# Performance work log

Measured on AMD Instinct MI355X. Metric: run time of the kernel, lower is better.

## Reference

```python
import jax, jax.numpy as jnp
import numpy as np

B, N, D_FEAT = 16, 1024, 64
NPOINT, RADIUS, NSAMPLE = 512, 0.2, 32
EPS = 1e-5


def _square_distance(src, dst):
    # src [b,S,3], dst [b,N,3] -> [b,S,N]
    d = -2.0 * jnp.einsum('bsc,bnc->bsn', src, dst)
    d = d + jnp.sum(src * src, -1)[:, :, None]
    d = d + jnp.sum(dst * dst, -1)[:, None, :]
    return d


def _fps(xyz, npoint):
    # xyz [b,N,3] -> indices [b,npoint]; seeded by point farthest from the mean
    b, n, _ = xyz.shape
    centroid = jnp.mean(xyz, axis=1, keepdims=True)
    distance = jnp.minimum(jnp.full((b, n), 1e10, xyz.dtype),
                           jnp.sum((xyz - centroid) ** 2, -1))
    farthest = jnp.argmax(distance, -1)
    bidx = jnp.arange(b)

    def body(carry, _):
        dist, far = carry
        c = xyz[bidx[:, None], far[:, None]]  # [b,1,3]
        dist = jnp.minimum(dist, jnp.sum((xyz - c) ** 2, -1))
        return (dist, jnp.argmax(dist, -1)), far

    _, idx = jax.lax.scan(body, (distance, farthest), None, length=npoint)
    return idx.T  # [b, npoint]


def _gather(points, idx):
    # points [b,N,C], idx [b,...] -> [b,...,C]
    return jax.vmap(lambda p, i: p[i])(points, idx)


def _query_ball(radius, nsample, xyz, new_xyz):
    # faithful to torch: mask out-of-radius with N, full sort, take first nsample,
    # replace sentinels by the first (closest-index) in-ball point
    b, n, _ = xyz.shape
    sqr = _square_distance(new_xyz, xyz)  # [b,S,N]
    idx = jnp.where(sqr > radius ** 2, n, jnp.arange(n)[None, None, :])
    idx = jnp.sort(idx, axis=-1)[:, :, :nsample]
    first = idx[:, :, :1]
    return jnp.where(idx == n, first, idx)


def _qbn(x):
    # QBN_RM training mode: divide by per-channel RMS of detached activations
    mean = jnp.mean(jax.lax.stop_gradient(x) ** 2, axis=(0, 2, 3))
    return x / jnp.sqrt(mean + EPS)[None, :, None, None]


def _qrelu(x):
    # scale each 3-vector by mod / max(mod, 1), coefficient detached
    b3, c, s, k = x.shape
    b = b3 // 3
    xd = jax.lax.stop_gradient(x).reshape(b, 3, c, s, k)
    mod = jnp.sqrt(jnp.sum(xd * xd, axis=1))  # [b,c,s,k]
    coeff = mod / jnp.maximum(mod, 1.0)
    return jnp.broadcast_to(coeff[:, None], (b, 3, c, s, k)).reshape(b3, c, s, k) * x


def _qmaxpool(x):
    # our_mpool1d with kernel (1, nsample): pick the max-modulus sample over K,
    # gather the same index for all 3 quaternion components
    b3, c, s, k = x.shape
    b = b3 // 3
    x5 = x.reshape(b, 3, c, s, k)
    mod = jnp.sum(jax.lax.stop_gradient(x5) ** 2, axis=1)  # argmax of mod == argmax of mod^2
    idx = jnp.argmax(mod, axis=-1)  # [b,c,s]
    idxb = jnp.broadcast_to(idx[:, None, :, :, None], (b, 3, c, s, 1))
    y = jnp.take_along_axis(x5, idxb, axis=-1)[..., 0]  # [b,3,c,s]
    return y.reshape(b3, c, s)


def setup_inputs() -> dict:
    key = jax.random.key(0)
    k1, k2, k3, k4, k5 = jax.random.split(key, 5)
    xyz = jax.random.normal(k1, (B, 3, N), dtype=jnp.float32)
    points = jax.random.normal(k2, (B * 3, D_FEAT, N), dtype=jnp.float32)
    W0 = jax.random.normal(k3, (64, 66), dtype=jnp.float32) * np.sqrt(2.0 / 66)
    W1 = jax.random.normal(k4, (64, 64), dtype=jnp.float32) * np.sqrt(2.0 / 64)
    W2 = jax.random.normal(k5, (128, 64), dtype=jnp.float32) * np.sqrt(2.0 / 64)
    return {"xyz": xyz, "points": points, "W0": W0, "W1": W1, "W2": W2}


def reference(xyz, points, W0, W1, W2):
    xyz_t = xyz.transpose(0, 2, 1)      # [B,N,3]
    pts_t = points.transpose(0, 2, 1)   # [B*3,N,D]

    fps_idx = _fps(xyz_t, NPOINT)                       # [B,S]
    new_xyz = _gather(xyz_t, fps_idx)                   # [B,S,3]
    idx = _query_ball(RADIUS, NSAMPLE, xyz_t, new_xyz)  # [B,S,K]

    g_xyz = _gather(xyz_t, idx)                         # [B,S,K,3]
    g_norm = g_xyz - new_xyz[:, :, None, :]
    gx = g_xyz.transpose(0, 3, 1, 2).reshape(B * 3, NPOINT, NSAMPLE, 1)
    gn = g_norm.transpose(0, 3, 1, 2).reshape(B * 3, NPOINT, NSAMPLE, 1)
    idx3 = jnp.broadcast_to(idx[:, None], (B, 3, NPOINT, NSAMPLE)).reshape(B * 3, NPOINT, NSAMPLE)
    gp = _gather(pts_t, idx3)                           # [B*3,S,K,D]

    x = jnp.concatenate([gn, gx, gp], axis=-1)          # [B*3,S,K,D+2]
    x = x.transpose(0, 3, 1, 2)                         # [B*3,D+2,S,K]
    for W in (W0, W1, W2):
        x = jnp.einsum('bcsk,oc->bosk', x, W)           # 1x1 conv, no bias
        x = _qrelu(_qbn(x))
    new_feat = _qmaxpool(x)                             # [B*3,128,S]
    return new_xyz.transpose(0, 2, 1), new_feat
```

## Files before the change

### kernel.cpp

```cpp
#include <hip/hip_runtime.h>

typedef unsigned int u32;
typedef unsigned long long u64;
typedef float v2f __attribute__((ext_vector_type(2)));

#define NB 16
#define NPT 1024
#define NP 512
#define NS 32
#define DF 64
#define RAD2 0.04f
#define EPSQ 1e-5f
#define CNTF 786432.0f
#define NGRP 8192
#define TCAP 96
#define TSLOT 128
#define NTILE_MAX 2731

__device__ __forceinline__ float rmul(float a, float b){ return __fmul_rn(a,b); }
__device__ __forceinline__ float radd(float a, float b){ return __fadd_rn(a,b); }
__device__ __forceinline__ float sq3(float a, float b, float c){
  return radd(radd(rmul(a,a), rmul(b,b)), rmul(c,c));
}

__device__ __forceinline__ float wave_sum64(float v){
  #pragma unroll
  for(int m=1;m<64;m<<=1) v += __shfl_xor(v, m, 64);
  return v;
}

__device__ __forceinline__ float half_sum32(float v){
  #pragma unroll
  for(int m=1;m<32;m<<=1) v += __shfl_xor(v, m, 64);
  return v;
}

#define DPPK(CTRL) do{ \
  unsigned _lo = (unsigned)k, _hi = (unsigned)(k>>32); \
  unsigned _mlo = (unsigned)__builtin_amdgcn_mov_dpp((int)_lo, (CTRL), 0xF, 0xF, true); \
  unsigned _mhi = (unsigned)__builtin_amdgcn_mov_dpp((int)_hi, (CTRL), 0xF, 0xF, true); \
  u64 _mk = ((u64)_mhi<<32) | _mlo; \
  k = (_mk > k) ? _mk : k; \
}while(0)

template<int PT>
__global__ __launch_bounds__(256) void fps_combo(const float* __restrict__ xyz,
                                                 float* __restrict__ out0,
                                                 const float* __restrict__ pts,
                                                 float* __restrict__ ptsT,
                                                 u32* __restrict__ witem){
#pragma clang fp contract(off)
  const int bid = blockIdx.x;
  const int t = threadIdx.x;
  if(bid >= 8){
    const int gid = (bid - 8)*256 + t;
    if(gid < NTILE_MAX*TSLOT) witem[gid] = 0xFFFFFFFFu;
    if constexpr(PT){
      const int w = gid >> 6, ln = gid & 63;
      if(w < 48*16){
        const int b3 = w >> 4, n0 = (w & 15) << 6;
        const float* src = pts + (((size_t)b3*64 + ln) << 10);
        float* dst = ptsT + (((size_t)b3*1024 + n0) << 6) + ln;
        #pragma unroll 4
        for(int i=0;i<64;i++) dst[(size_t)i << 6] = src[n0 + i];
      }
    }
    return;
  }
  __shared__ float4 plds[2048];
  if(t >= 64) return;
  const int lane = t;
  const int half = lane >> 5;
  const int hl   = lane & 31;
  const int b    = 2*bid + half;
  const float* xb = xyz + b*3*NPT;

  v2f px2[16], py2[16], pz2[16], dist2[16];
  u32 loj[32];
  #pragma unroll
  for(int i=0;i<16;i++){
    const int n0 = 64*i + hl, n1 = n0 + 32;
    float x0v = xb[n0],        x1v = xb[n1];
    float y0v = xb[NPT+n0],    y1v = xb[NPT+n1];
    float z0v = xb[2*NPT+n0],  z1v = xb[2*NPT+n1];
    px2[i].x = x0v; px2[i].y = x1v;
    py2[i].x = y0v; py2[i].y = y1v;
    pz2[i].x = z0v; pz2[i].y = z1v;
    loj[2*i]   = 1023u - (u32)n0;
    loj[2*i+1] = 1023u - (u32)n1;
    plds[(half<<10) + n0] = make_float4(x0v, y0v, z0v, 0.f);
    plds[(half<<10) + n1] = make_float4(x1v, y1v, z1v, 0.f);
  }
  float sx=0.f, sy=0.f, sz=0.f;
  #pragma unroll
  for(int i=0;i<16;i++){
    sx += px2[i].x; sx += px2[i].y;
    sy += py2[i].x; sy += py2[i].y;
    sz += pz2[i].x; sz += pz2[i].y;
  }
  sx = half_sum32(sx); sy = half_sum32(sy); sz = half_sum32(sz);
  const float cx = sx/1024.f, cy = sy/1024.f, cz = sz/1024.f;
  {
    v2f cx2; cx2.x=cx; cx2.y=cx;
    v2f cy2; cy2.x=cy; cy2.y=cy;
    v2f cz2; cz2.x=cz; cz2.y=cz;
    #pragma unroll
    for(int i=0;i<16;i++){
      v2f dx = px2[i]-cx2, dy = py2[i]-cy2, dz = pz2[i]-cz2;
      v2f m1 = dx*dx, m2 = dy*dy, a1 = m1+m2, m3 = dz*dz, s2 = a1+m3;
      dist2[i].x = fminf(1e10f, s2.x);
      dist2[i].y = fminf(1e10f, s2.y);
    }
  }
  auto reduce2 = [&](int& fA, int& fB){
    u64 kk[16];
    #pragma unroll
    for(int i=0;i<16;i++){
      float a = dist2[i].x, bb = dist2[i].y;
      bool tk = bb > a;
      float dw = tk ? bb : a;
      u32   lw = tk ? loj[2*i+1] : loj[2*i];
      kk[i] = ((u64)__float_as_uint(dw)<<32) | lw;
    }
    #pragma unroll
    for(int i=0;i<8;i++){ u64 l=kk[2*i], r=kk[2*i+1]; kk[i] = (r>l)?r:l; }
    #pragma unroll
    for(int i=0;i<4;i++){ u64 l=kk[2*i], r=kk[2*i+1]; kk[i] = (r>l)?r:l; }
    #pragma unroll
    for(int i=0;i<2;i++){ u64 l=kk[2*i], r=kk[2*i+1]; kk[i] = (r>l)?r:l; }
    u64 k = (kk[1]>kk[0]) ? kk[1] : kk[0];
    DPPK(0xB1);
    DPPK(0x4E);
    DPPK(0x124);
    DPPK(0x128);
    DPPK(0x142);
    unsigned lo = (unsigned)k;
    fA = 1023 - __builtin_amdgcn_readlane((int)lo, 31);
    fB = 1023 - __builtin_amdgcn_readlane((int)lo, 63);
  };

  __asm__ volatile("s_waitcnt lgkmcnt(0)" ::: "memory");
  int farA, farB;
  reduce2(farA, farB);
  for(int it=0; it<NP; ++it){
    const int farv = (lane & 32) ? farB : farA;
    const float4 qv = plds[(half<<10) + farv];
    if(hl == 0){
      out0[(b*3+0)*NP + it] = qv.x;
      out0[(b*3+1)*NP + it] = qv.y;
      out0[(b*3+2)*NP + it] = qv.z;
    }
    v2f qx2; qx2.x=qv.x; qx2.y=qv.x;
    v2f qy2; qy2.x=qv.y; qy2.y=qv.y;
    v2f qz2; qz2.x=qv.z; qz2.y=qv.z;
    #pragma unroll
    for(int i=0;i<16;i++){
      v2f dx = px2[i]-qx2, dy = py2[i]-qy2, dz = pz2[i]-qz2;
      v2f m1 = dx*dx, m2 = dy*dy, a1 = m1+m2, m3 = dz*dz, s2 = a1+m3;
      dist2[i].x = fminf(dist2[i].x, s2.x);
      dist2[i].y = fminf(dist2[i].y, s2.y);
    }
    reduce2(farA, farB);
  }
}

__global__ __launch_bounds__(256) void ball_kernel(const float* __restrict__ xyz,
                                                   const float* __restrict__ out0,
                                                   int* __restrict__ idxb,
                                                   int* __restrict__ cntb){
  const int gw = (blockIdx.x * 256 + threadIdx.x) >> 6;
  const int lane = threadIdx.x & 63;
  const int b = gw >> 9;
  const int s = gw & 511;
  const float s0 = out0[(b*3+0)*NP + s];
  const float s1 = out0[(b*3+1)*NP + s];
  const float s2 = out0[(b*3+2)*NP + s];
  const float ss = sq3(s0,s1,s2);
  const float* xb = xyz + b*3*NPT;
  int base = 0;
  int* row = idxb + (b*NP + s)*NS;
  for(int chk=0; chk<16 && base<NS; ++chk){
    const int n = chk*64 + lane;
    float d0 = xb[n], d1 = xb[NPT+n], d2 = xb[2*NPT+n];
    float dd = sq3(d0,d1,d2);
    float p  = radd(radd(rmul(s0,d0), rmul(s1,d1)), rmul(s2,d2));
    float sqr = radd(radd(rmul(-2.0f,p), ss), dd);
    bool inc = !(sqr > RAD2);
    unsigned long long mask = __ballot(inc);
    if(inc){
      int slot = base + __popcll(mask & ((1ull<<lane)-1ull));
      if(slot < NS) row[slot] = n;
    }
    base += __popcll(mask);
  }
  if(lane==0) cntb[gw] = (base < NS) ? base : NS;
}

__global__ __launch_bounds__(1024) void pack_kernel(const int* __restrict__ cntb,
                                                    const int* __restrict__ idxb,
                                                    u32* __restrict__ witem,
                                                    int* __restrict__ ntile_dev){
  const int t = threadIdx.x;
  const int lane = t & 63;
  const int wv = t >> 6;
  int c[8]; int s0 = 0;
  #pragma unroll
  for(int i=0;i<8;i++){ c[i] = cntb[t*8+i]; s0 += c[i]; }
  int pre = s0;
  #pragma unroll
  for(int d=1; d<64; d<<=1){
    int v = __shfl_up(pre, d, 64);
    if(lane >= d) pre += v;
  }
  __shared__ int wsum[16];
  if(lane==63) wsum[wv] = pre;
  __syncthreads();
  int wo = 0;
  #pragma unroll
  for(int w=0;w<16;w++) if(w < wv) wo += wsum[w];
  int m = wo + pre - s0;
  if(t==1023) *ntile_dev = (wo + pre + TCAP - 1) / TCAP;
  #pragma unroll
  for(int i=0;i<8;i++){
    const int g = t*8+i; const int cc = c[i];
    const int tile = m / TCAP; const int slot = m - TCAP*tile;
    const int* row = idxb + g*NS;
    for(int j=0;j<cc;j++){
      witem[tile*TSLOT + slot + j] = (u32)((g<<15) | (j<<10) | row[j]);
    }
    m += cc;
  }
}

template<int DEPTH, int PT>
__global__ __launch_bounds__(384) void pass_kernel(
  const float* __restrict__ xyz, const float* __restrict__ ptsrc,
  const float* __restrict__ W0, const float* __restrict__ W1, const float* __restrict__ W2,
  const float* __restrict__ out0, const u32* __restrict__ witem,
  const int* __restrict__ cntb, const int* __restrict__ ntile_dev,
  const float* __restrict__ inv1, const float* __restrict__ inv2,
  float* __restrict__ part, float* __restrict__ out1)
{
  const int t = threadIdx.x;
  const int c3 = t >> 7;
  const int r  = t & 127;
  const int lane = t & 63;
  const int wv = t >> 6;
  const int bi = blockIdx.x;

  if(bi >= *ntile_dev) return;

  __shared__ float sq[3][128][17];
  __shared__ float wstat[6][128];
  for(int i=t; i<6*128; i+=384) (&wstat[0][0])[i] = 0.f;
  __syncthreads();

  const u32 w = witem[bi*TSLOT + r];
  const bool valid = (w != 0xFFFFFFFFu);
  const int bs = valid ? (int)(w >> 15) : 0;
  const int j  = valid ? (int)((w >> 10) & 31) : 1;
  const int n  = valid ? (int)(w & 1023) : 0;
  const int b = bs >> 9;
  const int s = bs & 511;
  const int b3 = b*3 + c3;
  const int cv = cntb[bs];
  const float wgt = valid ? ((j==0) ? (float)(33 - cv) : 1.0f) : 0.0f;

  const float gx = xyz[b3*NPT + n];
  const float cx = out0[b3*NP + s];
  float x0[66];
  x0[0] = gx - cx;
  x0[1] = gx;
  if constexpr(PT){
    const float4* pr4 = reinterpret_cast<const float4*>(ptsrc + (((size_t)b3<<10) + (size_t)n)*DF);
    #pragma unroll
    for(int q=0;q<16;q++){
      float4 v = pr4[q];
      x0[2+4*q] = v.x; x0[3+4*q] = v.y; x0[4+4*q] = v.z; x0[5+4*q] = v.w;
    }
  } else {
    const float* pr = ptsrc + ((size_t)b3*DF)*NPT + n;
    #pragma unroll
    for(int c=0;c<DF;c++) x0[2+c] = pr[(size_t)c*NPT];
  }

  float y1[64];
  #pragma unroll
  for(int ch=0; ch<4; ++ch){
    float acc[16];
    #pragma unroll
    for(int oo=0;oo<16;oo++){
      const int o = ch*16+oo;
      float a = 0.f;
      #pragma unroll
      for(int c=0;c<66;c++) a = fmaf(W0[o*66+c], x0[c], a);
      acc[oo] = a;
    }
    if constexpr(DEPTH == 1){
      #pragma unroll
      for(int oo=0;oo<16;oo++){
        float v = wave_sum64(acc[oo]*acc[oo]*wgt);
        if(lane==0) wstat[wv][ch*16+oo] += v;
      }
    } else {
      #pragma unroll
      for(int oo=0;oo<16;oo++){
        const int o = ch*16+oo;
        float xp = acc[oo] * inv1[o];
        acc[oo] = xp;
        sq[c3][r][oo] = xp*xp;
      }
      __syncthreads();
      #pragma unroll
      for(int oo=0;oo<16;oo++){
        float m2 = (sq[0][r][oo] + sq[1][r][oo]) + sq[2][r][oo];
        float mod = sqrtf(m2);
        float cf = (mod >= 1.f) ? 1.f : mod;
        y1[ch*16+oo] = cf * acc[oo];
      }
      __syncthreads();
    }
  }
  if constexpr(DEPTH == 1){
    __syncthreads();
    if(t < 64){
      float sv = 0.f;
      #pragma unroll
      for(int wq=0;wq<6;wq++) sv += wstat[wq][t];
      part[bi*64 + t] = sv;
    }
    return;
  }

  float y2[64];
  #pragma unroll
  for(int ch=0; ch<4; ++ch){
    float acc[16];
    #pragma unroll
    for(int oo=0;oo<16;oo++){
      const int o = ch*16+oo;
      float a = 0.f;
      #pragma unroll
      for(int c=0;c<64;c++) a = fmaf(W1[o*64+c], y1[c], a);
      acc[oo] = a;
    }
    if constexpr(DEPTH == 2){
      #pragma unroll
      for(int oo=0;oo<16;oo++){
        float v = wave_sum64(acc[oo]*acc[oo]*wgt);
        if(lane==0) wstat[wv][ch*16+oo] += v;
      }
    } else {
      #pragma unroll
      for(int oo=0;oo<16;oo++){
        const int o = ch*16+oo;
        float xp = acc[oo] * inv2[o];
        acc[oo] = xp;
        sq[c3][r][oo] = xp*xp;
      }
      __syncthreads();
      #pragma unroll
      for(int oo=0;oo<16;oo++){
        float m2 = (sq[0][r][oo] + sq[1][r][oo]) + sq[2][r][oo];
        float mod = sqrtf(m2);
        float cf = (mod >= 1.f) ? 1.f : mod;
        y2[ch*16+oo] = cf * acc[oo];
      }
      __syncthreads();
    }
  }
  if constexpr(DEPTH == 2){
    __syncthreads();
    if(t < 64){
      float sv = 0.f;
      #pragma unroll
      for(int wq=0;wq<6;wq++) sv += wstat[wq][t];
      part[bi*64 + t] = sv;
    }
    return;
  }

  #pragma unroll
  for(int ch=0; ch<8; ++ch){
    float a3[16];
    #pragma unroll
    for(int oo=0;oo<16;oo++){
      const int o = ch*16+oo;
      float a = 0.f;
      #pragma unroll
      for(int c=0;c<64;c++) a = fmaf(W2[o*64+c], y2[c], a);
      a3[oo] = a;
      sq[c3][r][oo] = a;
    }
    __syncthreads();
    if(c3 == 0){
      #pragma unroll
      for(int oo=0;oo<16;oo++){
        float a0 = sq[0][r][oo], a1 = sq[1][r][oo], a2 = sq[2][r][oo];
        float m2 = radd(radd(rmul(a0,a0), rmul(a1,a1)), rmul(a2,a2));
        float v = wave_sum64(m2*wgt);
        if(lane==0) wstat[wv][ch*16+oo] += v;
        if(valid && j==0){
          float bvv = m2; int bjj = 0;
          for(int jj=1; jj<cv; ++jj){
            float c0 = sq[0][r+jj][oo], c1 = sq[1][r+jj][oo], c2 = sq[2][r+jj][oo];
            float mm = radd(radd(rmul(c0,c0), rmul(c1,c1)), rmul(c2,c2));
            if(mm > bvv){ bvv = mm; bjj = jj; }
          }
          const int o = ch*16+oo;
          #pragma unroll
          for(int cc=0;cc<3;cc++){
            out1[(((size_t)(3*b+cc))*128 + o)*NP + s] = sq[cc][r+bjj][oo];
          }
        }
      }
    }
    __syncthreads();
  }
  if(t < 128){
    part[bi*128 + t] = wstat[0][t] + wstat[1][t];
  }
}

__global__ __launch_bounds__(256) void fin_kernel(const float* __restrict__ part,
                                                  const int* __restrict__ ntile_dev, int nch,
                                                  float* __restrict__ inv){
  const int o = blockIdx.x;
  const int t = threadIdx.x;
  const int nblk = *ntile_dev;
  float sum = 0.f;
  for(int i=t; i<nblk; i+=256) sum += part[(size_t)i*nch + o];
  sum = wave_sum64(sum);
  __shared__ float red[4];
  if((t&63)==0) red[t>>6] = sum;
  __syncthreads();
  if(t==0){
    float tot = (red[0]+red[1])+(red[2]+red[3]);
    inv[o] = 1.0f / sqrtf(tot/CNTF + EPSQ);
  }
}

__global__ __launch_bounds__(256) void fin3_scale(const float* __restrict__ part3,
                                                  const int* __restrict__ ntile_dev,
                                                  float* __restrict__ out){
  const int o = blockIdx.x;
  const int t = threadIdx.x;
  const int nblk = *ntile_dev;
  float sum = 0.f;
  for(int i=t; i<nblk; i+=256) sum += part3[(size_t)i*128 + o];
  sum = wave_sum64(sum);
  __shared__ float red[4];
  __shared__ float sinv;
  if((t&63)==0) red[t>>6] = sum;
  __syncthreads();
  if(t==0){
    float tot = (red[0]+red[1])+(red[2]+red[3]);
    sinv = 1.0f / sqrtf(tot/CNTF + EPSQ);
  }
  __syncthreads();
  const float iv = sinv;
  float* base = out + NB*3*NP;
  const size_t str = (size_t)128*NP;
  for(int idx=t; idx<NB*NP; idx+=256){
    const int b = idx >> 9, s = idx & 511;
    size_t i0 = ((size_t)(b*3)*128 + o)*NP + s;
    float a0 = base[i0] * iv;
    float a1 = base[i0+str] * iv;
    float a2 = base[i0+2*str] * iv;
    float m2 = (a0*a0 + a1*a1) + a2*a2;
    float mod = sqrtf(m2);
    float cf = (mod >= 1.f) ? 1.f : mod;
    base[i0] = cf*a0; base[i0+str] = cf*a1; base[i0+2*str] = cf*a2;
  }
}

extern "C" void kernel_launch(void* const* d_in, const int* in_sizes, int n_in,
                              void* d_out, int out_size, void* d_ws, size_t ws_size,
                              hipStream_t stream){
  const float* xyz = (const float*)d_in[0];
  const float* pts = (const float*)d_in[1];
  const float* W0  = (const float*)d_in[2];
  const float* W1  = (const float*)d_in[3];
  const float* W2  = (const float*)d_in[4];
  float* out = (float*)d_out;

  char* p = (char*)d_ws;
  auto carve = [&](size_t bytes)->char*{
    char* q = p; p += (bytes + 255) & ~(size_t)255; return q;
  };
  int*   idxb      = (int*)  carve((size_t)NGRP*NS*4);
  int*   cntb      = (int*)  carve((size_t)NGRP*4);
  u32*   witem     = (u32*)  carve((size_t)NTILE_MAX*TSLOT*4);
  int*   ntile_dev = (int*)  carve(256);
  float* part1     = (float*)carve((size_t)NTILE_MAX*64*4);
  float* part2     = (float*)carve((size_t)NTILE_MAX*64*4);
  float* part3     = (float*)carve((size_t)NTILE_MAX*128*4);
  float* inv1      = (float*)carve(64*4);
  float* inv2      = (float*)carve(64*4);
  float* inv3      = (float*)carve(128*4);
  size_t base_need = (size_t)(p - (char*)d_ws);
  float* ptsT      = (float*)p;
  const size_t pt_bytes = (size_t)48*1024*64*4;
  const bool use_pt = (ws_size >= base_need + pt_bytes);

  float* out1 = out + NB*3*NP;

  const int copyblk = (NTILE_MAX*TSLOT + 255)/256;
  if(use_pt) fps_combo<1><<<8 + copyblk, 256, 0, stream>>>(xyz, out, pts, ptsT, witem);
  else       fps_combo<0><<<8 + copyblk, 256, 0, stream>>>(xyz, out, pts, nullptr, witem);

  ball_kernel<<<2048, 256, 0, stream>>>(xyz, out, idxb, cntb);
  pack_kernel<<<1, 1024, 0, stream>>>(cntb, idxb, witem, ntile_dev);

  if(use_pt){
    pass_kernel<1,1><<<NTILE_MAX, 384, 0, stream>>>(xyz, ptsT, W0, W1, W2, out, witem, cntb, ntile_dev, nullptr, nullptr, part1, nullptr);
    fin_kernel<<<64, 256, 0, stream>>>(part1, ntile_dev, 64, inv1);
    pass_kernel<2,1><<<NTILE_MAX, 384, 0, stream>>>(xyz, ptsT, W0, W1, W2, out, witem, cntb, ntile_dev, inv1, nullptr, part2, nullptr);
    fin_kernel<<<64, 256, 0, stream>>>(part2, ntile_dev, 64, inv2);
    pass_kernel<3,1><<<NTILE_MAX, 384, 0, stream>>>(xyz, ptsT, W0, W1, W2, out, witem, cntb, ntile_dev, inv1, inv2, part3, out1);
  } else {
    pass_kernel<1,0><<<NTILE_MAX, 384, 0, stream>>>(xyz, pts, W0, W1, W2, out, witem, cntb, ntile_dev, nullptr, nullptr, part1, nullptr);
    fin_kernel<<<64, 256, 0, stream>>>(part1, ntile_dev, 64, inv1);
    pass_kernel<2,0><<<NTILE_MAX, 384, 0, stream>>>(xyz, pts, W0, W1, W2, out, witem, cntb, ntile_dev, inv1, nullptr, part2, nullptr);
    fin_kernel<<<64, 256, 0, stream>>>(part2, ntile_dev, 64, inv2);
    pass_kernel<3,0><<<NTILE_MAX, 384, 0, stream>>>(xyz, pts, W0, W1, W2, out, witem, cntb, ntile_dev, inv1, inv2, part3, out1);
  }
  fin3_scale<<<128, 256, 0, stream>>>(part3, ntile_dev, out);
}
```

Before: 777.7 us.

## Overlap speculative all-point ball query with FPS and select rows afterwards

The ball query now runs for every one of the 1024 input points per batch, inside the same launch as farthest-point sampling, so it overlaps the long serial FPS loop. FPS records the chosen point indices, and the pack kernel looks up the precomputed neighbour rows and counts by those indices. This removes the separate ball-query launch and its dependency on FPS completing. It also adds spinning 'heater' blocks that loop until FPS signals done or a timeout expires, and raises the FPS wave priority. In exchange it does twice the ball-query work, uses more workspace, and relies on a spin flag plus a timeout.

```diff
diff --git a/kernel.cpp b/kernel.cpp
--- a/kernel.cpp
+++ b/kernel.cpp
@@ -16,6 +16,9 @@
 #define TCAP 96
 #define TSLOT 128
 #define NTILE_MAX 2731
+#define NHEAT 600
+#define NBALLBLK 4096
+#define NFILLBLK 1366
 
 __device__ __forceinline__ float rmul(float a, float b){ return __fmul_rn(a,b); }
 __device__ __forceinline__ float radd(float a, float b){ return __fadd_rn(a,b); }
@@ -28,7 +31,6 @@
   for(int m=1;m<64;m<<=1) v += __shfl_xor(v, m, 64);
   return v;
 }
-
 __device__ __forceinline__ float half_sum32(float v){
   #pragma unroll
   for(int m=1;m<32;m<<=1) v += __shfl_xor(v, m, 64);
@@ -48,27 +50,81 @@
                                                  float* __restrict__ out0,
                                                  const float* __restrict__ pts,
                                                  float* __restrict__ ptsT,
-                                                 u32* __restrict__ witem){
+                                                 u32* __restrict__ witem,
+                                                 int* __restrict__ idxb_full,
+                                                 int* __restrict__ cnt_full,
+                                                 int* __restrict__ farIdx,
+                                                 int* __restrict__ flagp){
 #pragma clang fp contract(off)
   const int bid = blockIdx.x;
   const int t = threadIdx.x;
+
+  if(bid >= 8 + NHEAT){
+    if(bid < 8 + NHEAT + NBALLBLK){
+      const int row = (bid - 8 - NHEAT)*4 + (t>>6);
+      const int lane = t & 63;
+      const int b = row >> 10;
+      const int nc = row & 1023;
+      const float* xb = xyz + b*3*NPT;
+      const float s0 = xb[nc], s1 = xb[NPT+nc], s2 = xb[2*NPT+nc];
+      const float ss = sq3(s0,s1,s2);
+      int base = 0;
+      int* rowp = idxb_full + row*NS;
+      for(int chk=0; chk<16 && base<NS; ++chk){
+        const int n = chk*64 + lane;
+        float d0 = xb[n], d1 = xb[NPT+n], d2 = xb[2*NPT+n];
+        float dd = sq3(d0,d1,d2);
+        float p  = radd(radd(rmul(s0,d0), rmul(s1,d1)), rmul(s2,d2));
+        float sqr = radd(radd(rmul(-2.0f,p), ss), dd);
+        bool inc = !(sqr > RAD2);
+        u64 mask = __ballot(inc);
+        if(inc){
+          int slot = base + __popcll(mask & ((1ull<<lane)-1ull));
+          if(slot < NS) rowp[slot] = n;
+        }
+        base += __popcll(mask);
+      }
+      if(lane==0) cnt_full[row] = (base < NS) ? base : NS;
+    } else {
+      const int gid = (bid - 8 - NHEAT - NBALLBLK)*256 + t;
+      if(gid < NTILE_MAX*TSLOT) witem[gid] = 0xFFFFFFFFu;
+      if constexpr(PT){
+        const int w = gid >> 6, ln = gid & 63;
+        if(w < 48*16){
+          const int b3 = w >> 4, n0 = (w & 15) << 6;
+          const float* src = pts + (((size_t)b3*64 + ln) << 10);
+          float* dst = ptsT + (((size_t)b3*1024 + n0) << 6) + ln;
+          #pragma unroll 4
+          for(int i=0;i<64;i++) dst[(size_t)i << 6] = src[n0 + i];
+        }
+      }
+    }
+    return;
+  }
+
   if(bid >= 8){
-    const int gid = (bid - 8)*256 + t;
-    if(gid < NTILE_MAX*TSLOT) witem[gid] = 0xFFFFFFFFu;
-    if constexpr(PT){
-      const int w = gid >> 6, ln = gid & 63;
-      if(w < 48*16){
-        const int b3 = w >> 4, n0 = (w & 15) << 6;
-        const float* src = pts + (((size_t)b3*64 + ln) << 10);
-        float* dst = ptsT + (((size_t)b3*1024 + n0) << 6) + ln;
-        #pragma unroll 4
-        for(int i=0;i<64;i++) dst[(size_t)i << 6] = src[n0 + i];
-      }
-    }
+    if(t >= 64) return;
+    __builtin_amdgcn_s_setprio(0);
+    const u64 t0 = __builtin_amdgcn_s_memrealtime();
+    float a0 = 1.0f, a1 = 1.1f, a2 = 1.2f, a3 = 1.3f;
+    while(true){
+      #pragma unroll
+      for(int i=0;i<128;i++){
+        a0 = fmaf(a0, 1.0000001f, 1e-30f);
+        a1 = fmaf(a1, 0.9999999f, 1e-30f);
+        a2 = fmaf(a2, 1.0000002f, 1e-30f);
+        a3 = fmaf(a3, 0.9999998f, 1e-30f);
+      }
+      if(__hip_atomic_load(flagp, __ATOMIC_RELAXED, __HIP_MEMORY_SCOPE_AGENT) >= 8) break;
+      if(__builtin_amdgcn_s_memrealtime() - t0 > 120000ull) break;
+    }
+    __asm__ volatile("" :: "v"(a0), "v"(a1), "v"(a2), "v"(a3));
     return;
   }
+
   __shared__ float4 plds[2048];
   if(t >= 64) return;
+  __builtin_amdgcn_s_setprio(3);
   const int lane = t;
   const int half = lane >> 5;
   const int hl   = lane & 31;
@@ -149,6 +205,7 @@
       out0[(b*3+0)*NP + it] = qv.x;
       out0[(b*3+1)*NP + it] = qv.y;
       out0[(b*3+2)*NP + it] = qv.z;
+      farIdx[b*NP + it] = farv;
     }
     v2f qx2; qx2.x=qv.x; qx2.y=qv.x;
     v2f qy2; qy2.x=qv.y; qy2.y=qv.y;
@@ -162,50 +219,28 @@
     }
     reduce2(farA, farB);
   }
-}
-
-__global__ __launch_bounds__(256) void ball_kernel(const float* __restrict__ xyz,
-                                                   const float* __restrict__ out0,
-                                                   int* __restrict__ idxb,
-                                                   int* __restrict__ cntb){
-  const int gw = (blockIdx.x * 256 + threadIdx.x) >> 6;
-  const int lane = threadIdx.x & 63;
-  const int b = gw >> 9;
-  const int s = gw & 511;
-  const float s0 = out0[(b*3+0)*NP + s];
-  const float s1 = out0[(b*3+1)*NP + s];
-  const float s2 = out0[(b*3+2)*NP + s];
-  const float ss = sq3(s0,s1,s2);
-  const float* xb = xyz + b*3*NPT;
-  int base = 0;
-  int* row = idxb + (b*NP + s)*NS;
-  for(int chk=0; chk<16 && base<NS; ++chk){
-    const int n = chk*64 + lane;
-    float d0 = xb[n], d1 = xb[NPT+n], d2 = xb[2*NPT+n];
-    float dd = sq3(d0,d1,d2);
-    float p  = radd(radd(rmul(s0,d0), rmul(s1,d1)), rmul(s2,d2));
-    float sqr = radd(radd(rmul(-2.0f,p), ss), dd);
-    bool inc = !(sqr > RAD2);
-    unsigned long long mask = __ballot(inc);
-    if(inc){
-      int slot = base + __popcll(mask & ((1ull<<lane)-1ull));
-      if(slot < NS) row[slot] = n;
-    }
-    base += __popcll(mask);
-  }
-  if(lane==0) cntb[gw] = (base < NS) ? base : NS;
-}
-
-__global__ __launch_bounds__(1024) void pack_kernel(const int* __restrict__ cntb,
-                                                    const int* __restrict__ idxb,
+  if(t == 0) atomicAdd(flagp, 1);
+}
+
+__global__ __launch_bounds__(1024) void pack_kernel(const int* __restrict__ farIdx,
+                                                    const int* __restrict__ cnt_full,
+                                                    const int* __restrict__ idxb_full,
                                                     u32* __restrict__ witem,
-                                                    int* __restrict__ ntile_dev){
+                                                    int* __restrict__ ntile_dev,
+                                                    int* __restrict__ cntb){
   const int t = threadIdx.x;
   const int lane = t & 63;
   const int wv = t >> 6;
-  int c[8]; int s0 = 0;
-  #pragma unroll
-  for(int i=0;i<8;i++){ c[i] = cntb[t*8+i]; s0 += c[i]; }
+  int c[8]; int rowid[8]; int s0 = 0;
+  #pragma unroll
+  for(int i=0;i<8;i++){
+    const int g = t*8+i;
+    const int far = farIdx[g];
+    rowid[i] = ((g>>9)<<10) + far;
+    c[i] = cnt_full[rowid[i]];
+    cntb[g] = c[i];
+    s0 += c[i];
+  }
   int pre = s0;
   #pragma unroll
   for(int d=1; d<64; d<<=1){
@@ -224,9 +259,9 @@
   for(int i=0;i<8;i++){
     const int g = t*8+i; const int cc = c[i];
     const int tile = m / TCAP; const int slot = m - TCAP*tile;
-    const int* row = idxb + g*NS;
+    const int* rp = idxb_full + rowid[i]*NS;
     for(int j=0;j<cc;j++){
-      witem[tile*TSLOT + slot + j] = (u32)((g<<15) | (j<<10) | row[j]);
+      witem[tile*TSLOT + slot + j] = (u32)((g<<15) | (j<<10) | rp[j]);
     }
     m += cc;
   }
@@ -488,7 +523,10 @@
   auto carve = [&](size_t bytes)->char*{
     char* q = p; p += (bytes + 255) & ~(size_t)255; return q;
   };
-  int*   idxb      = (int*)  carve((size_t)NGRP*NS*4);
+  int*   idxb_full = (int*)  carve((size_t)NB*NPT*NS*4);
+  int*   cnt_full  = (int*)  carve((size_t)NB*NPT*4);
+  int*   farIdx    = (int*)  carve((size_t)NGRP*4);
+  int*   flagp     = (int*)  carve(256);
   int*   cntb      = (int*)  carve((size_t)NGRP*4);
   u32*   witem     = (u32*)  carve((size_t)NTILE_MAX*TSLOT*4);
   int*   ntile_dev = (int*)  carve(256);
@@ -504,13 +542,13 @@
   const bool use_pt = (ws_size >= base_need + pt_bytes);
 
   float* out1 = out + NB*3*NP;
-
-  const int copyblk = (NTILE_MAX*TSLOT + 255)/256;
-  if(use_pt) fps_combo<1><<<8 + copyblk, 256, 0, stream>>>(xyz, out, pts, ptsT, witem);
-  else       fps_combo<0><<<8 + copyblk, 256, 0, stream>>>(xyz, out, pts, nullptr, witem);
-
-  ball_kernel<<<2048, 256, 0, stream>>>(xyz, out, idxb, cntb);
-  pack_kernel<<<1, 1024, 0, stream>>>(cntb, idxb, witem, ntile_dev);
+  const int nblk = 8 + NHEAT + NBALLBLK + NFILLBLK;
+
+  hipMemsetAsync(flagp, 0, 4, stream);
+  if(use_pt) fps_combo<1><<<nblk, 256, 0, stream>>>(xyz, out, pts, ptsT, witem, idxb_full, cnt_full, farIdx, flagp);
+  else       fps_combo<0><<<nblk, 256, 0, stream>>>(xyz, out, pts, nullptr, witem, idxb_full, cnt_full, farIdx, flagp);
+
+  pack_kernel<<<1, 1024, 0, stream>>>(farIdx, cnt_full, idxb_full, witem, ntile_dev, cntb);
 
   if(use_pt){
     pass_kernel<1,1><<<NTILE_MAX, 384, 0, stream>>>(xyz, ptsT, W0, W1, W2, out, witem, cntb, ntile_dev, nullptr, nullptr, part1, nullptr);
```

New measurement: 789.2 us. Within noise of the previous version (+1.5%).
